# Kernel optimization log

Measured on AMD Instinct MI355X. Metric: run time of the kernel, lower is better.

## Reference

```python
import jax, jax.numpy as jnp
import numpy as np

IN_FEATURES = 256
WIDTH = 512
GRID_POINTS = 32   # num control points
DEGREE = 3         # spline_order
BATCH = 8192
LN_EPS = 1e-5


def make_knots(num_ctrl_pts, degree):
    knot_count = num_ctrl_pts + degree + 1
    knots = np.zeros(knot_count, dtype=np.float32)
    knots[-(degree + 1):] = 1.0
    interior = knot_count - 2 * (degree + 1)
    if interior > 0:
        knots[degree + 1:degree + 1 + interior] = np.linspace(0.0, 1.0, interior + 2, dtype=np.float32)[1:-1]
    return jnp.asarray(knots)

KNOTS = make_knots(GRID_POINTS, DEGREE)  # [num_ctrl + degree + 1]


def bspline_basis(x, knots, degree):
    # x: [b, f] in [0,1]; returns [b, f, num_ctrl_pts]
    xe = x[..., None]                      # [b, f, 1]
    left = knots[:-1]
    right = knots[1:]
    basis = ((xe >= left) & (xe < right)).astype(x.dtype)            # [b,f,K-1]
    last = ((xe >= left[-1]) & (xe <= right[-1])).astype(x.dtype)    # [b,f,1]
    basis = jnp.concatenate([basis[..., :-1], last], axis=-1)
    for r in range(1, degree + 1):  # fixed small loop over spline order
        m = basis.shape[-1] - 1
        if m <= 0:
            break
        idx = np.arange(m)
        lk = knots[idx]                 # [m]
        rk = knots[idx + r + 1]
        d1 = knots[idx + r] - knots[idx]
        d2 = knots[idx + r + 1] - knots[idx + 1]
        s1 = jnp.where(d1 > 0, d1, 1.0)  # safe denominators (avoid nan in both where branches)
        s2 = jnp.where(d2 > 0, d2, 1.0)
        t1 = jnp.where(d1 > 0, (xe - lk) / s1, 0.0) * basis[..., :m]
        t2 = jnp.where(d2 > 0, (rk - xe) / s2, 0.0) * basis[..., 1:m + 1]
        basis = t1 + t2
    return basis


def setup_inputs() -> dict:
    key = jax.random.key(0)
    ks = jax.random.split(key, 8)
    coeff_init = np.sqrt(2.0 / (GRID_POINTS * IN_FEATURES)).astype(np.float32)
    return {
        "inputs": jax.random.normal(ks[0], (BATCH, IN_FEATURES), dtype=jnp.float32),
        "input_shift": jnp.zeros((IN_FEATURES,), dtype=jnp.float32),
        "input_log_scale": jnp.zeros((IN_FEATURES,), dtype=jnp.float32),
        "spline_coeffs": coeff_init * jax.random.normal(ks[1], (IN_FEATURES, GRID_POINTS, WIDTH), dtype=jnp.float32),
        "bias": jnp.zeros((WIDTH,), dtype=jnp.float32),
        "skip_w": jax.random.normal(ks[2], (IN_FEATURES, WIDTH), dtype=jnp.float32) / np.sqrt(IN_FEATURES).astype(np.float32),
        "skip_b": jnp.zeros((WIDTH,), dtype=jnp.float32),
        "ln_gamma": jnp.ones((WIDTH,), dtype=jnp.float32),
        "ln_beta": jnp.zeros((WIDTH,), dtype=jnp.float32),
    }


def reference(inputs, input_shift, input_log_scale, spline_coeffs, bias,
              skip_w, skip_b, ln_gamma, ln_beta):
    scale = jax.nn.softplus(input_log_scale) + 0.001
    normalised = jax.nn.sigmoid((inputs - input_shift) * scale)            # [b,f] in (0,1)
    basis = bspline_basis(normalised, KNOTS, DEGREE)                       # [b,f,g]
    spline_mix = jnp.einsum('bfg,fgw->bw', basis, spline_coeffs)
    linear_skip = inputs @ skip_w + skip_b
    combined = spline_mix + linear_skip + bias
    mu = jnp.mean(combined, axis=-1, keepdims=True)
    var = jnp.mean(jnp.square(combined - mu), axis=-1, keepdims=True)
    normed = (combined - mu) * jax.lax.rsqrt(var + LN_EPS) * ln_gamma + ln_beta
    return jax.nn.gelu(normed, approximate=False)  # torch nn.GELU default = exact erf
```

## Files before the change

kernel.cpp:

```cpp
#include <hip/hip_runtime.h>
#include <hip/hip_bf16.h>
#include <math.h>

#define BATCH 8192
#define F 256
#define G 32
#define W 512
#define NCHUNK 132
#define NPER 66

typedef float f32x4 __attribute__((ext_vector_type(4)));
typedef short s16x8 __attribute__((ext_vector_type(8)));
typedef long long i64x2 __attribute__((ext_vector_type(2)));

__device__ __forceinline__ short f2bf(float f) {
  unsigned int u = __builtin_bit_cast(unsigned int, f);
  u += 0x7fffu + ((u >> 16) & 1u);
  return (short)(u >> 16);
}

__device__ __forceinline__ float knotv(int i) {
  int j = i - 3;
  j = j < 0 ? 0 : (j > 29 ? 29 : j);
  return (float)j * (1.0f / 29.0f);
}

__device__ __forceinline__ float fdiv_fast(float a, float b) {
  return a * __builtin_amdgcn_rcpf(b);
}

__global__ __launch_bounds__(256) void bws_build(
    const float* __restrict__ coeffs, const float* __restrict__ skip_w,
    short* __restrict__ Bws)
{
  const int gid = blockIdx.x * 256 + threadIdx.x;
  const int lane = gid & 63;
  const int kk = (gid >> 6) & 1;
  const int nf = (gid >> 7) & 3;
  const int wn = (gid >> 9) & 1;
  const int nt = (gid >> 10) & 3;
  const int c  = gid >> 12;
  const int w  = nt * 128 + wn * 64 + nf * 16 + (lane & 15);
  const int kl = kk * 32 + (lane >> 4) * 8;
  const float* src = (c < 128) ? (coeffs + (size_t)(c * 64 + kl) * W + w)
                               : (skip_w + (size_t)((c - 128) * 64 + kl) * W + w);
  s16x8 h;
  #pragma unroll
  for (int j = 0; j < 8; ++j) h[j] = f2bf(src[(size_t)j * W]);
  ((s16x8*)Bws)[gid] = h;
}

__device__ __forceinline__ void stage_period(short* __restrict__ Ab, int p,
    int tid, int m0, const unsigned short* __restrict__ sgl,
    const float* __restrict__ inp)
{
  const int ci = tid >> 7;
  const int hi = (tid >> 6) & 1;
  const int bp = tid & 63;
  const int cc = 2 * p + ci;
  const int mf = bp >> 4, l15b = bp & 15;
  short* base = Ab + ci * 4096 + ((mf * 2 + hi) * 64 + l15b) * 8;
  if (cc < 128) {
    const float sg = ((float)sgl[(2 * cc + hi) * 64 + bp] + 0.5f) * (1.0f / 65536.0f);
    const int s0 = (int)(sg * 29.0f);
    const int sp = s0 + 3;
    float Nv[4], lef[4], rig[4];
    Nv[0] = 1.0f;
    #pragma unroll
    for (int r = 1; r <= 3; ++r) {
      lef[r] = sg - knotv(sp + 1 - r);
      rig[r] = knotv(sp + r) - sg;
      float saved = 0.0f;
      #pragma unroll
      for (int j = 0; j < r; ++j) {
        float temp = fdiv_fast(Nv[j], rig[j + 1] + lef[r - j]);
        Nv[j] = saved + rig[j + 1] * temp;
        saved = lef[r - j] * temp;
      }
      Nv[r] = saved;
    }
    unsigned long long nv =
        (unsigned long long)(unsigned short)f2bf(Nv[0])
      | ((unsigned long long)(unsigned short)f2bf(Nv[1]) << 16)
      | ((unsigned long long)(unsigned short)f2bf(Nv[2]) << 32)
      | ((unsigned long long)(unsigned short)f2bf(Nv[3]) << 48);
    const int pp = s0 & 7, ga = s0 >> 3;
    const int s = 16 * pp, shl = s & 63;
    const unsigned long long a = nv << shl;
    const unsigned long long b = (nv >> (63 - shl)) >> 1;
    const bool hs = (s >= 64);
    i64x2 d0, d1, z;
    d0[0] = hs ? 0ll : (long long)a;
    d0[1] = hs ? (long long)a : (long long)b;
    d1[0] = hs ? (long long)b : 0ll;
    d1[1] = 0ll;
    z[0] = 0ll; z[1] = 0ll;
    *(i64x2*)(base + ga * 128) = d0;
    *(i64x2*)(base + ((ga + 1) & 3) * 128) = d1;
    *(i64x2*)(base + ((ga + 2) & 3) * 128) = z;
    *(i64x2*)(base + ((ga + 3) & 3) * 128) = z;
  } else {
    const int sb = (cc - 128) * 64 + hi * 32;
    const float* ip = inp + (size_t)(m0 + bp) * F + sb;
    #pragma unroll
    for (int lq = 0; lq < 4; ++lq) {
      s16x8 h;
      #pragma unroll
      for (int j = 0; j < 8; ++j) h[j] = f2bf(ip[lq * 8 + j]);
      *(s16x8*)(base + lq * 128) = h;
    }
  }
}

__global__ __launch_bounds__(256, 2) void kan_gemm_v6(
    const float* __restrict__ inp, const float* __restrict__ shift,
    const float* __restrict__ lscale, const short* __restrict__ Bws,
    const float* __restrict__ bias, const float* __restrict__ skip_b,
    float* __restrict__ out)
{
  __shared__ short Abuf[2][8192];
  __shared__ unsigned short sgl[F * 64];
  __shared__ float shf[2 * F];

  const int tid = threadIdx.x;
  const int lane = tid & 63;
  const int wn = tid >> 6;

  const int nb = (blockIdx.x & 7) * 64 + (blockIdx.x >> 3);
  const int mt = nb >> 2, nt = nb & 3;
  const int m0 = mt * 64, n0 = nt * 128;

  {
    float ls = lscale[tid];
    shf[tid] = fmaxf(ls, 0.0f) + __logf(1.0f + __expf(-fabsf(ls))) + 0.001f;
    shf[256 + tid] = shift[tid];
  }
  __syncthreads();

  {
    const int row = lane;
    const int qc = wn;
    const float* ip = inp + (size_t)(m0 + row) * F + qc * 64;
    #pragma unroll
    for (int i = 0; i < 16; ++i) {
      float4 v = *(const float4*)(ip + i * 4);
      float vv[4] = {v.x, v.y, v.z, v.w};
      #pragma unroll
      for (int j = 0; j < 4; ++j) {
        const int f = qc * 64 + i * 4 + j;
        const float z = (vv[j] - shf[256 + f]) * shf[f];
        const float sg = 1.0f / (1.0f + __expf(-z));
        sgl[f * 64 + row] = (unsigned short)fminf(sg * 65536.0f, 65535.0f);
      }
    }
  }
  __syncthreads();

  f32x4 acc[4][2];
  #pragma unroll
  for (int i = 0; i < 4; ++i)
    #pragma unroll
    for (int j = 0; j < 2; ++j)
      acc[i][j] = (f32x4){0.f, 0.f, 0.f, 0.f};

  const int wnB = wn >> 1, lo = wn & 1;
  const short* bq0 = Bws + (size_t)(nt * 16 + wnB * 8 + lo * 4) * 512 + lane * 8;
  const short* bq1 = bq0 + 32768;

#define LOADB(BS) do {                                                          \
    _Pragma("unroll")                                                           \
    for (int nf = 0; nf < 2; ++nf)                                              \
      _Pragma("unroll")                                                         \
      for (int kk = 0; kk < 2; ++kk) {                                          \
        BS[0 * 4 + nf * 2 + kk] = *(const s16x8*)(bq0 + nf * 1024 + kk * 512);  \
        BS[1 * 4 + nf * 2 + kk] = *(const s16x8*)(bq1 + nf * 1024 + kk * 512);  \
      }                                                                         \
    bq0 += 65536; bq1 += 65536;                                                 \
  } while (0)

#define MMAC(AB, BS)                                                            \
    _Pragma("unroll")                                                           \
    for (int ci = 0; ci < 2; ++ci)                                              \
      _Pragma("unroll")                                                         \
      for (int kk = 0; kk < 2; ++kk)                                            \
        _Pragma("unroll")                                                       \
        for (int mf = 0; mf < 4; ++mf) {                                        \
          s16x8 af = *(const s16x8*)&AB[ci * 4096 + ((mf * 2 + kk) * 64 + lane) * 8]; \
          _Pragma("unroll")                                                     \
          for (int nf = 0; nf < 2; ++nf)                                        \
            acc[mf][nf] = __builtin_amdgcn_mfma_f32_16x16x32_bf16(              \
                af, BS[ci * 4 + nf * 2 + kk], acc[mf][nf], 0, 0, 0);            \
        }

#define PERIOD(P_, ACUR, ANXT, BCUR, BNXT) do {                                 \
    asm volatile("s_waitcnt lgkmcnt(0)" ::: "memory");                          \
    __builtin_amdgcn_s_barrier();                                               \
    if ((P_) + 1 < NPER) LOADB(BNXT);                                           \
    __builtin_amdgcn_s_setprio(1);                                              \
    MMAC(ACUR, BCUR);                                                           \
    __builtin_amdgcn_s_setprio(0);                                              \
    if ((P_) + 1 < NPER) stage_period(ANXT, (P_) + 1, tid, m0, sgl, inp);       \
  } while (0)

  s16x8 bA[8], bB[8];
  LOADB(bA);
  stage_period(&Abuf[0][0], 0, tid, m0, sgl, inp);

  for (int p = 0; p < NPER; p += 2) {
    PERIOD(p,     Abuf[0], (&Abuf[1][0]), bA, bB);
    PERIOD(p + 1, Abuf[1], (&Abuf[0][0]), bB, bA);
  }
#undef PERIOD
#undef MMAC
#undef LOADB

  const int l15 = lane & 15;
  const int lq = lane >> 4;
  #pragma unroll
  for (int nf = 0; nf < 2; ++nf) {
    const int col = n0 + wn * 32 + nf * 16 + l15;
    const float badd = bias[col] + skip_b[col];
    #pragma unroll
    for (int mf = 0; mf < 4; ++mf) {
      const int r0 = m0 + mf * 16 + lq * 4;
      #pragma unroll
      for (int r = 0; r < 4; ++r)
        out[(size_t)(r0 + r) * W + col] = acc[mf][nf][r] + badd;
    }
  }
}

__device__ __forceinline__ void issue_b(int c, int uu, int n0,
                                        const float* __restrict__ coeffs,
                                        const float* __restrict__ skip_w,
                                        float (&r)[4][8]) {
  const float* base = (c < 128) ? (coeffs + (size_t)c * 64 * W)
                                : (skip_w + (size_t)(c - 128) * 64 * W);
  const int kk = (uu >> 6) & 1;
  const int lq = (uu >> 4) & 3;
  const int l15 = uu & 15;
  const int u7 = uu >> 7;
  #pragma unroll
  for (int s = 0; s < 4; ++s) {
    const int w = (2 * s + u7) * 16 + l15;
    const float* p = base + (size_t)(kk * 32 + lq * 8) * W + n0 + w;
    #pragma unroll
    for (int j = 0; j < 8; ++j) r[s][j] = p[(size_t)j * W];
  }
}

__global__ __launch_bounds__(512, 1) void kan_gemm_v2(
    const float* __restrict__ inp, const float* __restrict__ shift,
    const float* __restrict__ lscale, const float* __restrict__ coeffs,
    const float* __restrict__ bias, const float* __restrict__ skip_w,
    const float* __restrict__ skip_b, float* __restrict__ out)
{
  __shared__ short Abuf[2][8192];
  __shared__ short Bbuf[2][8192];
  __shared__ unsigned short sgl[F * 128];

  const int tid = threadIdx.x;
  const int lane = tid & 63;
  const int wid = tid >> 6;
  const int nb = (blockIdx.x & 7) * 32 + (blockIdx.x >> 3);
  const int mt = nb >> 2;
  const int nt = nb & 3;
  const int m0 = mt * 128;
  const int n0 = nt * 128;

  float bpref[4][8];
  if (tid >= 256) issue_b(0, tid - 256, n0, coeffs, skip_w, bpref);

  float* shf = (float*)&Abuf[0][0];
  if (tid < 256) {
    float ls = lscale[tid];
    shf[tid] = fmaxf(ls, 0.0f) + __logf(1.0f + __expf(-fabsf(ls))) + 0.001f;
    shf[256 + tid] = shift[tid];
  }
  __syncthreads();

  {
    const int row = tid & 127;
    const int q = tid >> 7;
    const float* ip = inp + (size_t)(m0 + row) * F + q * 64;
    #pragma unroll
    for (int i = 0; i < 16; ++i) {
      float4 v = *(const float4*)(ip + i * 4);
      float vv[4] = {v.x, v.y, v.z, v.w};
      #pragma unroll
      for (int j = 0; j < 4; ++j) {
        const int f = q * 64 + i * 4 + j;
        const float z = (vv[j] - shf[256 + f]) * shf[f];
        const float sg = 1.0f / (1.0f + __expf(-z));
        sgl[f * 128 + row] = (unsigned short)fminf(sg * 65536.0f, 65535.0f);
      }
    }
  }
  __syncthreads();

  const int wm = wid >> 2;
  const int wn = wid & 3;

  f32x4 acc[4][2];
  #pragma unroll
  for (int i = 0; i < 4; ++i)
    #pragma unroll
    for (int j = 0; j < 2; ++j)
      acc[i][j] = (f32x4){0.f, 0.f, 0.f, 0.f};

  for (int c = 0; c < NCHUNK; ++c) {
    short* Ab = Abuf[c & 1];
    short* Bb = Bbuf[c & 1];

    if (c < 128) {
      s16x8 z = {0, 0, 0, 0, 0, 0, 0, 0};
      ((s16x8*)Ab)[tid * 2] = z;
      ((s16x8*)Ab)[tid * 2 + 1] = z;
    } else if (tid < 256) {
      const int bp = tid & 127, fi = tid >> 7;
      const int sb = (c - 128) * 64 + fi * 32;
      const float* ip = inp + (size_t)(m0 + bp) * F + sb;
      const int rg = bp >> 4, l15b = bp & 15;
      #pragma unroll
      for (int lq2 = 0; lq2 < 4; ++lq2) {
        s16x8 h;
        #pragma unroll
        for (int j = 0; j < 8; ++j) h[j] = f2bf(ip[lq2 * 8 + j]);
        *(s16x8*)&Ab[((rg * 2 + fi) * 64 + lq2 * 16 + l15b) * 8] = h;
      }
    }
    if (tid >= 256) {
      const int uu = tid - 256;
      #pragma unroll
      for (int s = 0; s < 4; ++s) {
        s16x8 h;
        #pragma unroll
        for (int j = 0; j < 8; ++j) h[j] = f2bf(bpref[s][j]);
        *(s16x8*)&Bb[(s * 256 + uu) * 8] = h;
      }
      if (c + 1 < NCHUNK) issue_b(c + 1, uu, n0, coeffs, skip_w, bpref);
    }
    __syncthreads();

    if (c < 128 && tid < 256) {
      const int bp = tid & 127, fi = tid >> 7;
      const int f = 2 * c + fi;
      const float sg = ((float)sgl[f * 128 + bp] + 0.5f) * (1.0f / 65536.0f);
      int s0 = (int)floorf(sg * 29.0f);
      s0 = s0 < 0 ? 0 : (s0 > 28 ? 28 : s0);
      const int sp = s0 + 3;
      float Nv[4], lef[4], rig[4];
      Nv[0] = 1.0f;
      #pragma unroll
      for (int r = 1; r <= 3; ++r) {
        lef[r] = sg - knotv(sp + 1 - r);
        rig[r] = knotv(sp + r) - sg;
        float saved = 0.0f;
        #pragma unroll
        for (int j = 0; j < r; ++j) {
          float temp = fdiv_fast(Nv[j], rig[j + 1] + lef[r - j]);
          Nv[j] = saved + rig[j + 1] * temp;
          saved = lef[r - j] * temp;
        }
        Nv[r] = saved;
      }
      const int rg = bp >> 4, l15b = bp & 15;
      #pragma unroll
      for (int t = 0; t < 4; ++t) {
        const int g = s0 + t;
        Ab[((rg * 2 + fi) * 64 + (g >> 3) * 16 + l15b) * 8 + (g & 7)] = f2bf(Nv[t]);
      }
    }
    s16x8 bfv[2][2];
    #pragma unroll
    for (int nf = 0; nf < 2; ++nf)
      #pragma unroll
      for (int kk = 0; kk < 2; ++kk)
        bfv[nf][kk] = *(const s16x8*)&Bb[(((wn * 2 + nf) * 2 + kk) * 64 + lane) * 8];
    __syncthreads();

    #pragma unroll
    for (int kk = 0; kk < 2; ++kk) {
      #pragma unroll
      for (int mf = 0; mf < 4; ++mf) {
        s16x8 af = *(const s16x8*)&Ab[(((wm * 4 + mf) * 2 + kk) * 64 + lane) * 8];
        #pragma unroll
        for (int nf = 0; nf < 2; ++nf)
          acc[mf][nf] = __builtin_amdgcn_mfma_f32_16x16x32_bf16(af, bfv[nf][kk], acc[mf][nf], 0, 0, 0);
      }
    }
  }

  const int l15 = lane & 15;
  const int lq = lane >> 4;
  #pragma unroll
  for (int nf = 0; nf < 2; ++nf) {
    const int col = n0 + wn * 32 + nf * 16 + l15;
    const float badd = bias[col] + skip_b[col];
    #pragma unroll
    for (int mf = 0; mf < 4; ++mf) {
      const int r0 = m0 + wm * 64 + mf * 16 + lq * 4;
      #pragma unroll
      for (int r = 0; r < 4; ++r)
        out[(size_t)(r0 + r) * W + col] = acc[mf][nf][r] + badd;
    }
  }
}

__global__ __launch_bounds__(256, 1) void ln_gelu(
    float* __restrict__ out, const float* __restrict__ gamma,
    const float* __restrict__ beta)
{
  const int lane = threadIdx.x & 63;
  const int wid = threadIdx.x >> 6;
  const int row = blockIdx.x * 4 + wid;
  float* p = out + (size_t)row * W + lane * 8;
  float4 a = *(const float4*)p;
  float4 b = *(const float4*)(p + 4);
  float v[8] = {a.x, a.y, a.z, a.w, b.x, b.y, b.z, b.w};
  float s = 0.f, q = 0.f;
  #pragma unroll
  for (int j = 0; j < 8; ++j) { s += v[j]; q += v[j] * v[j]; }
  #pragma unroll
  for (int m = 1; m < 64; m <<= 1) {
    s += __shfl_xor(s, m);
    q += __shfl_xor(q, m);
  }
  const float mu = s * (1.0f / 512.0f);
  const float var = q * (1.0f / 512.0f) - mu * mu;
  const float inv = rsqrtf(var + 1e-5f);
  const float4 g0 = *(const float4*)(gamma + lane * 8);
  const float4 g1 = *(const float4*)(gamma + lane * 8 + 4);
  const float4 b0 = *(const float4*)(beta + lane * 8);
  const float4 b1 = *(const float4*)(beta + lane * 8 + 4);
  float gm[8] = {g0.x, g0.y, g0.z, g0.w, g1.x, g1.y, g1.z, g1.w};
  float bt[8] = {b0.x, b0.y, b0.z, b0.w, b1.x, b1.y, b1.z, b1.w};
  float o[8];
  #pragma unroll
  for (int j = 0; j < 8; ++j) {
    float x = (v[j] - mu) * inv * gm[j] + bt[j];
    o[j] = 0.5f * x * (1.0f + erff(x * 0.70710678f));
  }
  float4 w0 = {o[0], o[1], o[2], o[3]};
  float4 w1 = {o[4], o[5], o[6], o[7]};
  *(float4*)p = w0;
  *(float4*)(p + 4) = w1;
}

extern "C" void kernel_launch(void* const* d_in, const int* in_sizes, int n_in,
                              void* d_out, int out_size, void* d_ws, size_t ws_size,
                              hipStream_t stream) {
  (void)in_sizes; (void)n_in; (void)out_size;
  const float* inp    = (const float*)d_in[0];
  const float* shift  = (const float*)d_in[1];
  const float* lscale = (const float*)d_in[2];
  const float* coeffs = (const float*)d_in[3];
  const float* bias   = (const float*)d_in[4];
  const float* skip_w = (const float*)d_in[5];
  const float* skip_b = (const float*)d_in[6];
  const float* gamma  = (const float*)d_in[7];
  const float* beta   = (const float*)d_in[8];
  float* out = (float*)d_out;

  const size_t needB = (size_t)NCHUNK * 4 * 16384;

  if (ws_size >= needB) {
    short* Bws = (short*)d_ws;
    bws_build<<<dim3(2112), dim3(256), 0, stream>>>(coeffs, skip_w, Bws);
    kan_gemm_v6<<<dim3(512), dim3(256), 0, stream>>>(
        inp, shift, lscale, Bws, bias, skip_b, out);
  } else {
    kan_gemm_v2<<<dim3(256), dim3(512), 0, stream>>>(
        inp, shift, lscale, coeffs, bias, skip_w, skip_b, out);
  }
  ln_gelu<<<dim3(BATCH / 4), dim3(256), 0, stream>>>(out, gamma, beta);
}
```

Before: 107.7 us.

## Precompute packed B-spline basis in separate kernel and prefetch into GEMM pipeline

Adds a bas_build kernel that computes the sigmoid, knot span and four packed bf16 basis values for every (feature, batch) element and writes them to workspace. The GEMM kernel no longer computes sigmoids into LDS or runs the Cox-de Boor recursion per period. It instead prefetches the precomputed values two periods ahead from global memory and only scatters them into the A tile. This takes ALU work and an LDS prologue off the MFMA critical path and frees shared memory. The cost is an extra kernel launch plus roughly 18 MB of extra global traffic, and the basis is now recomputed by 4 N-tiles' worth of readers hitting cache.

```diff
diff --git a/kernel.cpp b/kernel.cpp
--- a/kernel.cpp
+++ b/kernel.cpp
@@ -27,6 +27,64 @@
 
 __device__ __forceinline__ float fdiv_fast(float a, float b) {
   return a * __builtin_amdgcn_rcpf(b);
+}
+
+__global__ __launch_bounds__(256) void bas_build(
+    const float* __restrict__ inp, const float* __restrict__ shift,
+    const float* __restrict__ lscale,
+    unsigned long long* __restrict__ nvq, unsigned char* __restrict__ s0q)
+{
+  __shared__ float T[64][257];
+  const int b0 = blockIdx.x * 64;
+  const int t = threadIdx.x;
+  {
+    const int r = t & 63, q = t >> 6;
+    const float* src = inp + (size_t)(b0 + r) * F + q * 64;
+    #pragma unroll
+    for (int i = 0; i < 16; ++i) {
+      float4 v = *(const float4*)(src + i * 4);
+      T[r][q * 64 + i * 4 + 0] = v.x;
+      T[r][q * 64 + i * 4 + 1] = v.y;
+      T[r][q * 64 + i * 4 + 2] = v.z;
+      T[r][q * 64 + i * 4 + 3] = v.w;
+    }
+  }
+  __syncthreads();
+  const int f = t;
+  float ls = lscale[f];
+  const float sc = fmaxf(ls, 0.0f) + __logf(1.0f + __expf(-fabsf(ls))) + 0.001f;
+  const float sh = shift[f];
+  unsigned long long* nd = nvq + (size_t)f * BATCH + b0;
+  unsigned char* sd = s0q + (size_t)f * BATCH + b0;
+  for (int rr = 0; rr < 64; ++rr) {
+    const float z = (T[rr][f] - sh) * sc;
+    const float sg = 1.0f / (1.0f + __expf(-z));
+    int s0 = (int)(sg * 29.0f);
+    s0 = s0 < 0 ? 0 : (s0 > 28 ? 28 : s0);
+    const int sp = s0 + 3;
+    float Nv[4], lef[4], rig[4];
+    Nv[0] = 1.0f;
+    #pragma unroll
+    for (int r = 1; r <= 3; ++r) {
+      lef[r] = sg - knotv(sp + 1 - r);
+      rig[r] = knotv(sp + r) - sg;
+      float saved = 0.0f;
+      #pragma unroll
+      for (int j = 0; j < r; ++j) {
+        float temp = fdiv_fast(Nv[j], rig[j + 1] + lef[r - j]);
+        Nv[j] = saved + rig[j + 1] * temp;
+        saved = lef[r - j] * temp;
+      }
+      Nv[r] = saved;
+    }
+    const unsigned long long nv =
+        (unsigned long long)(unsigned short)f2bf(Nv[0])
+      | ((unsigned long long)(unsigned short)f2bf(Nv[1]) << 16)
+      | ((unsigned long long)(unsigned short)f2bf(Nv[2]) << 32)
+      | ((unsigned long long)(unsigned short)f2bf(Nv[3]) << 48);
+    nd[rr] = nv;
+    sd[rr] = (unsigned char)s0;
+  }
 }
 
 __global__ __launch_bounds__(256) void bws_build(
@@ -50,40 +108,12 @@
   ((s16x8*)Bws)[gid] = h;
 }
 
-__device__ __forceinline__ void stage_period(short* __restrict__ Ab, int p,
-    int tid, int m0, const unsigned short* __restrict__ sgl,
-    const float* __restrict__ inp)
+__device__ __forceinline__ void stage_nv(short* __restrict__ Ab, int cc,
+    int stoff, int hi, int bp, int m0,
+    unsigned long long nv, int s0, const float* __restrict__ inp)
 {
-  const int ci = tid >> 7;
-  const int hi = (tid >> 6) & 1;
-  const int bp = tid & 63;
-  const int cc = 2 * p + ci;
-  const int mf = bp >> 4, l15b = bp & 15;
-  short* base = Ab + ci * 4096 + ((mf * 2 + hi) * 64 + l15b) * 8;
+  short* base = Ab + stoff;
   if (cc < 128) {
-    const float sg = ((float)sgl[(2 * cc + hi) * 64 + bp] + 0.5f) * (1.0f / 65536.0f);
-    const int s0 = (int)(sg * 29.0f);
-    const int sp = s0 + 3;
-    float Nv[4], lef[4], rig[4];
-    Nv[0] = 1.0f;
-    #pragma unroll
-    for (int r = 1; r <= 3; ++r) {
-      lef[r] = sg - knotv(sp + 1 - r);
-      rig[r] = knotv(sp + r) - sg;
-      float saved = 0.0f;
-      #pragma unroll
-      for (int j = 0; j < r; ++j) {
-        float temp = fdiv_fast(Nv[j], rig[j + 1] + lef[r - j]);
-        Nv[j] = saved + rig[j + 1] * temp;
-        saved = lef[r - j] * temp;
-      }
-      Nv[r] = saved;
-    }
-    unsigned long long nv =
-        (unsigned long long)(unsigned short)f2bf(Nv[0])
-      | ((unsigned long long)(unsigned short)f2bf(Nv[1]) << 16)
-      | ((unsigned long long)(unsigned short)f2bf(Nv[2]) << 32)
-      | ((unsigned long long)(unsigned short)f2bf(Nv[3]) << 48);
     const int pp = s0 & 7, ga = s0 >> 3;
     const int s = 16 * pp, shl = s & 63;
     const unsigned long long a = nv << shl;
@@ -112,15 +142,13 @@
   }
 }
 
-__global__ __launch_bounds__(256, 2) void kan_gemm_v6(
-    const float* __restrict__ inp, const float* __restrict__ shift,
-    const float* __restrict__ lscale, const short* __restrict__ Bws,
+__global__ __launch_bounds__(256, 2) void kan_gemm_v8(
+    const float* __restrict__ inp, const short* __restrict__ Bws,
+    const unsigned long long* __restrict__ nvq, const unsigned char* __restrict__ s0q,
     const float* __restrict__ bias, const float* __restrict__ skip_b,
     float* __restrict__ out)
 {
   __shared__ short Abuf[2][8192];
-  __shared__ unsigned short sgl[F * 64];
-  __shared__ float shf[2 * F];
 
   const int tid = threadIdx.x;
   const int lane = tid & 63;
@@ -130,31 +158,11 @@
   const int mt = nb >> 2, nt = nb & 3;
   const int m0 = mt * 64, n0 = nt * 128;
 
-  {
-    float ls = lscale[tid];
-    shf[tid] = fmaxf(ls, 0.0f) + __logf(1.0f + __expf(-fabsf(ls))) + 0.001f;
-    shf[256 + tid] = shift[tid];
-  }
-  __syncthreads();
-
-  {
-    const int row = lane;
-    const int qc = wn;
-    const float* ip = inp + (size_t)(m0 + row) * F + qc * 64;
-    #pragma unroll
-    for (int i = 0; i < 16; ++i) {
-      float4 v = *(const float4*)(ip + i * 4);
-      float vv[4] = {v.x, v.y, v.z, v.w};
-      #pragma unroll
-      for (int j = 0; j < 4; ++j) {
-        const int f = qc * 64 + i * 4 + j;
-        const float z = (vv[j] - shf[256 + f]) * shf[f];
-        const float sg = 1.0f / (1.0f + __expf(-z));
-        sgl[f * 64 + row] = (unsigned short)fminf(sg * 65536.0f, 65535.0f);
-      }
-    }
-  }
-  __syncthreads();
+  const int ci = tid >> 7;
+  const int hi = (tid >> 6) & 1;
+  const int bp = tid & 63;
+  const int mg = bp >> 4, l15b = bp & 15;
+  const int stoff = ci * 4096 + ((mg * 2 + hi) * 64 + l15b) * 8;
 
   f32x4 acc[4][2];
   #pragma unroll
@@ -178,40 +186,58 @@
     bq0 += 65536; bq1 += 65536;                                                 \
   } while (0)
 
+#define PREF(NVL, S0L, PTGT) do {                                               \
+    const int cc_ = 2 * (PTGT) + ci;                                            \
+    if ((PTGT) < NPER && cc_ < 128) {                                           \
+      const size_t ix_ = (size_t)(2 * cc_ + hi) * BATCH + m0 + bp;              \
+      NVL = nvq[ix_];                                                           \
+      S0L = s0q[ix_];                                                           \
+    }                                                                           \
+  } while (0)
+
 #define MMAC(AB, BS)                                                            \
     _Pragma("unroll")                                                           \
-    for (int ci = 0; ci < 2; ++ci)                                              \
+    for (int cj = 0; cj < 2; ++cj)                                              \
       _Pragma("unroll")                                                         \
       for (int kk = 0; kk < 2; ++kk)                                            \
         _Pragma("unroll")                                                       \
         for (int mf = 0; mf < 4; ++mf) {                                        \
-          s16x8 af = *(const s16x8*)&AB[ci * 4096 + ((mf * 2 + kk) * 64 + lane) * 8]; \
+          s16x8 af = *(const s16x8*)&AB[cj * 4096 + ((mf * 2 + kk) * 64 + lane) * 8]; \
           _Pragma("unroll")                                                     \
           for (int nf = 0; nf < 2; ++nf)                                        \
             acc[mf][nf] = __builtin_amdgcn_mfma_f32_16x16x32_bf16(              \
-                af, BS[ci * 4 + nf * 2 + kk], acc[mf][nf], 0, 0, 0);            \
+                af, BS[cj * 4 + nf * 2 + kk], acc[mf][nf], 0, 0, 0);            \
         }
 
-#define PERIOD(P_, ACUR, ANXT, BCUR, BNXT) do {                                 \
+#define PERIOD(P_, ACUR, ANXT, BCUR, BNXT, NVU, S0U, NVL, S0L) do {             \
     asm volatile("s_waitcnt lgkmcnt(0)" ::: "memory");                          \
     __builtin_amdgcn_s_barrier();                                               \
-    if ((P_) + 1 < NPER) LOADB(BNXT);                                           \
+    PREF(NVL, S0L, (P_) + 2);                                                   \
+    if ((P_) + 1 < NPER) {                                                      \
+      LOADB(BNXT);                                                              \
+      stage_nv(ANXT, 2 * ((P_) + 1) + ci, stoff, hi, bp, m0, NVU, S0U, inp);    \
+    }                                                                           \
     __builtin_amdgcn_s_setprio(1);                                              \
     MMAC(ACUR, BCUR);                                                           \
     __builtin_amdgcn_s_setprio(0);                                              \
-    if ((P_) + 1 < NPER) stage_period(ANXT, (P_) + 1, tid, m0, sgl, inp);       \
   } while (0)
 
   s16x8 bA[8], bB[8];
+  unsigned long long nvA = 0, nvB = 0;
+  int s0A = 0, s0B = 0;
+
+  PREF(nvA, s0A, 0);
   LOADB(bA);
-  stage_period(&Abuf[0][0], 0, tid, m0, sgl, inp);
+  stage_nv(&Abuf[0][0], 2 * 0 + ci, stoff, hi, bp, m0, nvA, s0A, inp);
+  PREF(nvB, s0B, 1);
 
   for (int p = 0; p < NPER; p += 2) {
-    PERIOD(p,     Abuf[0], (&Abuf[1][0]), bA, bB);
-    PERIOD(p + 1, Abuf[1], (&Abuf[0][0]), bB, bA);
+    PERIOD(p,     (&Abuf[0][0]), (&Abuf[1][0]), bA, bB, nvB, s0B, nvA, s0A);
+    PERIOD(p + 1, (&Abuf[1][0]), (&Abuf[0][0]), bB, bA, nvA, s0A, nvB, s0B);
   }
 #undef PERIOD
 #undef MMAC
+#undef PREF
 #undef LOADB
 
   const int l15 = lane & 15;
@@ -462,13 +488,18 @@
   const float* beta   = (const float*)d_in[8];
   float* out = (float*)d_out;
 
-  const size_t needB = (size_t)NCHUNK * 4 * 16384;
-
-  if (ws_size >= needB) {
+  const size_t needB  = (size_t)NCHUNK * 4 * 16384;
+  const size_t needNV = (size_t)F * BATCH * 8;
+  const size_t needS0 = (size_t)F * BATCH;
+
+  if (ws_size >= needB + needNV + needS0) {
     short* Bws = (short*)d_ws;
+    unsigned long long* nvq = (unsigned long long*)((char*)d_ws + needB);
+    unsigned char* s0q = (unsigned char*)((char*)d_ws + needB + needNV);
+    bas_build<<<dim3(BATCH / 64), dim3(256), 0, stream>>>(inp, shift, lscale, nvq, s0q);
     bws_build<<<dim3(2112), dim3(256), 0, stream>>>(coeffs, skip_w, Bws);
-    kan_gemm_v6<<<dim3(512), dim3(256), 0, stream>>>(
-        inp, shift, lscale, Bws, bias, skip_b, out);
+    kan_gemm_v8<<<dim3(512), dim3(256), 0, stream>>>(
+        inp, Bws, nvq, s0q, bias, skip_b, out);
   } else {
     kan_gemm_v2<<<dim3(256), dim3(512), 0, stream>>>(
         inp, shift, lscale, coeffs, bias, skip_w, skip_b, out);
```

Result: slower. 120.9 us (+12.3%).
